# Performance work log

Measured on AMD Instinct MI355X. Metric: run time of the kernel, lower is better.

The kernel has to match this reference:

```python
import jax, jax.numpy as jnp
import numpy as np
import math

D = 1024
B, S = 4, 4096


def setup_inputs() -> dict:
    key = jax.random.key(0)
    ks = jax.random.split(key, 8)
    x = jax.random.normal(ks[0], (B, S, D), dtype=jnp.float32)
    W_omega = jax.random.normal(ks[1], (D, D), dtype=jnp.float32) * (1.0 / math.sqrt(D))
    b_omega = jnp.zeros((D,), dtype=jnp.float32)
    log_scale = jnp.full((D,), math.log(0.1), dtype=jnp.float32)
    ln_gamma = jnp.ones((4 * D,), dtype=jnp.float32)
    ln_beta = jnp.zeros((4 * D,), dtype=jnp.float32)
    W1 = jax.random.normal(ks[2], (4 * D, 2 * D), dtype=jnp.float32) * (1.0 / math.sqrt(4 * D))
    b1 = jnp.zeros((2 * D,), dtype=jnp.float32)
    W2 = jax.random.normal(ks[3], (2 * D, D), dtype=jnp.float32) * (1.0 / math.sqrt(2 * D))
    b2 = jnp.zeros((D,), dtype=jnp.float32)
    return {"x": x, "W_omega": W_omega, "b_omega": b_omega, "log_scale": log_scale,
            "ln_gamma": ln_gamma, "ln_beta": ln_beta, "W1": W1, "b1": b1, "W2": W2, "b2": b2}


def _layernorm(x, gamma, beta, eps=1e-5):
    mu = jnp.mean(x, axis=-1, keepdims=True)
    var = jnp.var(x, axis=-1, keepdims=True)
    return (x - mu) * jax.lax.rsqrt(var + eps) * gamma + beta


def reference(x, W_omega, b_omega, log_scale, ln_gamma, ln_beta, W1, b1, W2, b2):
    # x: (B, S, D)
    seq_len = x.shape[1]
    omega = jnp.einsum('bsd,de->bse', x, W_omega) + b_omega
    position = jnp.arange(1, seq_len + 1, dtype=x.dtype)[None, :, None]  # (1,S,1)
    pos_scale = 1.0 / jnp.sqrt(position)
    scale = jnp.exp(log_scale)
    omega_scaled = omega * scale * pos_scale
    phi = jnp.cumsum(omega_scaled, axis=1)
    cos_phi = jnp.cos(phi)
    sin_phi = jnp.sin(phi)
    content_real = x * cos_phi
    content_imag = x * sin_phi
    mem_real = jnp.cumsum(content_real, axis=1) / position
    mem_imag = jnp.cumsum(content_imag, axis=1) / position
    retrieved_real = mem_real * cos_phi + mem_imag * sin_phi
    retrieved_imag = mem_imag * cos_phi - mem_real * sin_phi
    context = jnp.concatenate([content_real, content_imag, retrieved_real, retrieved_imag], axis=-1)
    h = _layernorm(context, ln_gamma, ln_beta)
    h = jnp.einsum('bsf,fg->bsg', h, W1) + b1
    h = jax.nn.gelu(h, approximate=False)  # torch GELU default is exact erf
    # dropout is identity in eval mode
    phase_contribution = jnp.einsum('bsg,gd->bsd', h, W2) + b2
    return x + phase_contribution
```

## Files before the change

### kernel.cpp

```cpp
#include <hip/hip_runtime.h>
#include <hip/hip_bf16.h>
#include <math.h>

typedef __hip_bfloat16 bf16;
typedef __attribute__((ext_vector_type(8))) short bf16x8;
typedef __attribute__((ext_vector_type(4))) float f32x4;

static constexpr int DD = 1024;
static constexpr int BB = 4;
static constexpr int SS = 4096;
static constexpr int FD = 4096;
static constexpr int GDIM = 2048;
static constexpr long SD = (long)SS * DD;
static constexpr long SD4 = 4 * SD;

__device__ __forceinline__ void gl2lds16(const bf16* g, bf16* l) {
    __builtin_amdgcn_global_load_lds(
        (const __attribute__((address_space(1))) void*)g,
        (__attribute__((address_space(3))) void*)l, 16, 0, 0);
}

__device__ __forceinline__ float gelu_exact(float v) {
    const float ax = fabsf(v) * 0.70710678118654752f;
    const float t = 1.0f / (1.0f + 0.3275911f * ax);
    const float poly = t * (0.254829592f + t * (-0.284496736f +
                       t * (1.421413741f + t * (-1.453152027f + t * 1.061405429f))));
    const float er = 1.0f - poly * __expf(-ax * ax);
    const float erfv = v < 0.f ? -er : er;
    return 0.5f * v * (1.0f + erfv);
}

__device__ __forceinline__ float bf2f(unsigned short us) {
    return __uint_as_float(((unsigned)us) << 16);
}

template <int EPI>
__global__ __launch_bounds__(512, 2) void gemm256(
    const bf16* __restrict__ A, const bf16* __restrict__ BT, void* __restrict__ Cp,
    const float* __restrict__ bias, const float* __restrict__ Xadd,
    const float2* __restrict__ is2, const float* __restrict__ uArr,
    const float* __restrict__ tArr,
    int M, int N, int K, long strA, long strBT, long strC)
{
    extern __shared__ bf16 lds[];
    const int tid = threadIdx.x;
    const int l = tid & 63, wv = tid >> 6;
    const int wr = wv >> 2, wc = wv & 3;

    int lin = blockIdx.y * gridDim.x + blockIdx.x;
    {
        const int nwg = gridDim.x * gridDim.y;
        const int qq = nwg >> 3, rr = nwg & 7;
        const int xcd = lin & 7, idx = lin >> 3;
        lin = (xcd < rr ? xcd * (qq + 1) : rr * (qq + 1) + (xcd - rr) * qq) + idx;
    }
    const long m0 = (long)(lin / gridDim.x) * 256;
    const long n0 = (long)(lin % gridDim.x) * 256;

    A += (long)blockIdx.z * strA;
    BT += (long)blockIdx.z * strBT;

    const int schunk = (tid & 3) ^ ((tid >> 3) & 3);
    const bf16* pa = A + (m0 + (tid >> 2)) * (long)K + schunk * 8;
    const bf16* pb = BT + (n0 + (tid >> 2)) * (long)K + schunk * 8;
    const long rowK = 128L * (long)K;
    const int stgOff = wv * 512;

    const int fm = l & 15, q = l >> 4;
    const int lof = fm * 32 + ((q ^ ((fm >> 1) & 3)) * 8);

    f32x4 acc[8][4];
#pragma unroll
    for (int i = 0; i < 8; ++i)
#pragma unroll
        for (int j = 0; j < 4; ++j) acc[i][j] = (f32x4){0.f, 0.f, 0.f, 0.f};

    const int NT = K >> 6;

    {
        bf16* dA0 = lds + stgOff;
        bf16* dA1 = lds + 8192 + stgOff;
        bf16* dB0 = lds + 32768 + stgOff;
        bf16* dB1 = lds + 40960 + stgOff;
        gl2lds16(pa, dA0);       gl2lds16(pa + rowK, dA0 + 4096);
        gl2lds16(pb, dB0);       gl2lds16(pb + rowK, dB0 + 4096);
        gl2lds16(pa + 32, dA1);  gl2lds16(pa + 32 + rowK, dA1 + 4096);
        gl2lds16(pb + 32, dB1);  gl2lds16(pb + 32 + rowK, dB1 + 4096);
        asm volatile("s_waitcnt vmcnt(4)" ::: "memory");
        __builtin_amdgcn_s_barrier();
    }

    for (int t = 0; t < NT; ++t) {
        const int buf = t & 1;
        const bool more = (t + 1) < NT;
        const long ko = (long)(t + 1) * 64;
        const bf16* As0 = lds + buf * 16384;
        const bf16* As1 = As0 + 8192;
        const bf16* Bs0 = lds + 32768 + buf * 16384;
        const bf16* Bs1 = Bs0 + 8192;
        bf16* nA0 = lds + (buf ^ 1) * 16384 + stgOff;
        bf16* nA1 = nA0 + 8192;
        bf16* nB0 = lds + 32768 + (buf ^ 1) * 16384 + stgOff;
        bf16* nB1 = nB0 + 8192;

        {
            const bf16* bb = Bs0 + (wc * 64) * 32 + lof;
            const bf16* ab = As0 + (wr * 128) * 32 + lof;
            bf16x8 bq[4], a0[4], a1[4];
#pragma unroll
            for (int j = 0; j < 4; ++j) bq[j] = *(const bf16x8*)(bb + j * 512);
#pragma unroll
            for (int i = 0; i < 4; ++i) a0[i] = *(const bf16x8*)(ab + i * 512);
#pragma unroll
            for (int i = 0; i < 4; ++i) a1[i] = *(const bf16x8*)(ab + 64 * 32 + i * 512);
            if (more) {
                gl2lds16(pa + ko, nA0); gl2lds16(pa + ko + rowK, nA0 + 4096);
                gl2lds16(pb + ko, nB0); gl2lds16(pb + ko + rowK, nB0 + 4096);
            }
            __builtin_amdgcn_s_setprio(1);
#pragma unroll
            for (int i = 0; i < 4; ++i)
#pragma unroll
                for (int j = 0; j < 4; ++j)
                    acc[i][j] = __builtin_amdgcn_mfma_f32_16x16x32_bf16(a0[i], bq[j], acc[i][j], 0, 0, 0);
            __builtin_amdgcn_s_setprio(0);
            if (more) { gl2lds16(pa + ko + 32, nA1); gl2lds16(pa + ko + 32 + rowK, nA1 + 4096); }
            __builtin_amdgcn_s_setprio(1);
#pragma unroll
            for (int i = 0; i < 4; ++i)
#pragma unroll
                for (int j = 0; j < 4; ++j)
                    acc[4 + i][j] = __builtin_amdgcn_mfma_f32_16x16x32_bf16(a1[i], bq[j], acc[4 + i][j], 0, 0, 0);
            __builtin_amdgcn_s_setprio(0);
        }
        if (more) asm volatile("s_waitcnt vmcnt(6)" ::: "memory");
        else      asm volatile("s_waitcnt vmcnt(0)" ::: "memory");
        __builtin_amdgcn_s_barrier();

        {
            const bf16* bb = Bs1 + (wc * 64) * 32 + lof;
            const bf16* ab = As1 + (wr * 128) * 32 + lof;
            bf16x8 bq[4], a0[4], a1[4];
#pragma unroll
            for (int j = 0; j < 4; ++j) bq[j] = *(const bf16x8*)(bb + j * 512);
#pragma unroll
            for (int i = 0; i < 4; ++i) a0[i] = *(const bf16x8*)(ab + i * 512);
#pragma unroll
            for (int i = 0; i < 4; ++i) a1[i] = *(const bf16x8*)(ab + 64 * 32 + i * 512);
            if (more) { gl2lds16(pb + ko + 32, nB1); gl2lds16(pb + ko + 32 + rowK, nB1 + 4096); }
            __builtin_amdgcn_s_setprio(1);
#pragma unroll
            for (int i = 0; i < 4; ++i)
#pragma unroll
                for (int j = 0; j < 4; ++j)
                    acc[i][j] = __builtin_amdgcn_mfma_f32_16x16x32_bf16(a0[i], bq[j], acc[i][j], 0, 0, 0);
            __builtin_amdgcn_s_setprio(0);
            __builtin_amdgcn_s_setprio(1);
#pragma unroll
            for (int i = 0; i < 4; ++i)
#pragma unroll
                for (int j = 0; j < 4; ++j)
                    acc[4 + i][j] = __builtin_amdgcn_mfma_f32_16x16x32_bf16(a1[i], bq[j], acc[4 + i][j], 0, 0, 0);
            __builtin_amdgcn_s_setprio(0);
        }
        if (more) {
            asm volatile("s_waitcnt vmcnt(4)" ::: "memory");
            __builtin_amdgcn_s_barrier();
        }
    }

    const long cb = (long)blockIdx.z * strC;
    float uu[4], tb[4];
    if (EPI == 1) {
#pragma unroll
        for (int j = 0; j < 4; ++j) {
            const long col = n0 + wc * 64 + j * 16 + fm;
            uu[j] = uArr[col];
            tb[j] = tArr[col] + bias[col];
        }
    }
#pragma unroll
    for (int i = 0; i < 8; ++i) {
        const long rB = m0 + wr * 128 + i * 16 + q * 4;
#pragma unroll
        for (int r2 = 0; r2 < 4; ++r2) {
            const long row = rB + r2;
            float2 st;
            if (EPI == 1) st = is2[row];
#pragma unroll
            for (int j = 0; j < 4; ++j) {
                const long col = n0 + wc * 64 + j * 16 + fm;
                float v = acc[i][j][r2];
                if (EPI == 0) {
                    v += bias[row];
                    ((bf16*)Cp)[cb + row * (long)N + col] = __float2bfloat16(v);
                } else if (EPI == 1) {
                    v = st.x * v - st.y * uu[j] + tb[j];
                    v = gelu_exact(v);
                    ((bf16*)Cp)[cb + row * (long)N + col] = __float2bfloat16(v);
                } else {
                    v += bias[col] + Xadd[row * (long)N + col];
                    ((float*)Cp)[cb + row * (long)N + col] = v;
                }
            }
        }
    }
}

__global__ void conv_bf16(const float* __restrict__ in, bf16* __restrict__ out, long n) {
    long i = ((long)blockIdx.x * 256 + threadIdx.x) * 4;
    if (i >= n) return;
    const float4 v = *(const float4*)(in + i);
    bf16 o[4] = {__float2bfloat16(v.x), __float2bfloat16(v.y),
                 __float2bfloat16(v.z), __float2bfloat16(v.w)};
    *(uint2*)(out + i) = *(uint2*)o;
}

__global__ void transpose_f32_bf16(const float* __restrict__ in, bf16* __restrict__ out,
                                   int R, int C, long inStr, long outStr,
                                   const float* __restrict__ rscale) {
    __shared__ float tl[64][65];
    const float* ip = in + (long)blockIdx.z * inStr;
    bf16* op = out + (long)blockIdx.z * outStr;
    const int r0 = blockIdx.y * 64, c0 = blockIdx.x * 64;
    const int tr = threadIdx.x >> 6, tc = threadIdx.x & 63;
#pragma unroll
    for (int k = 0; k < 16; k++) {
        int r = k * 4 + tr;
        float v = ip[(long)(r0 + r) * C + c0 + tc];
        if (rscale) v *= rscale[r0 + r];
        tl[r][tc] = v;
    }
    __syncthreads();
#pragma unroll
    for (int k = 0; k < 16; k++) {
        int r = k * 4 + tr;
        op[(long)(c0 + r) * R + r0 + tc] = __float2bfloat16(tl[tc][r]);
    }
}

__global__ void zero_f32(float* p, int n) {
    int i = blockIdx.x * 256 + threadIdx.x;
    if (i < n) p[i] = 0.f;
}

__global__ void ut_kernel(const float* __restrict__ W1, const float* __restrict__ gamma,
                          const float* __restrict__ beta, float* __restrict__ uArr,
                          float* __restrict__ tArr) {
    const int g = blockIdx.x * 256 + threadIdx.x;
    const int f0 = blockIdx.y * 512;
    float su = 0.f, st = 0.f;
    for (int f = 0; f < 512; ++f) {
        const float w = W1[(long)(f0 + f) * GDIM + g];
        su += gamma[f0 + f] * w;
        st += beta[f0 + f] * w;
    }
    atomicAdd(&uArr[g], su);
    atomicAdd(&tArr[g], st);
}

__global__ __launch_bounds__(512) void scan8(
    const bf16* __restrict__ omegaT, const bf16* __restrict__ xT,
    const float* __restrict__ log_scale, bf16* __restrict__ ctx,
    long strIn, long strCtx)
{
    __shared__ float stA[8], stB[8], stC[8];
    const int d = blockIdx.x;
    const int z = blockIdx.z;
    const int wv = threadIdx.x >> 6, lane = threadIdx.x & 63;
    const float sc = expf(log_scale[d]);
    const bf16* po = omegaT + (long)z * strIn + (long)d * SS;
    const bf16* px = xT + (long)z * strIn + (long)d * SS;
    bf16* pc = ctx + (long)z * strCtx + (long)d * SS;

    const int s0 = wv * 512;
    float phi_loc[8], xv[8], cph[8], sph[8], crs[8], cis[8];

    float lphi = 0.f;
#pragma unroll
    for (int c = 0; c < 8; ++c) {
        const int s = s0 + c * 64 + lane;
        const float pos = (float)(s + 1);
        float w = __bfloat162float(po[s]) * sc * rsqrtf(pos);
        xv[c] = __bfloat162float(px[s]);
#pragma unroll
        for (int dlt = 1; dlt < 64; dlt <<= 1) {
            float v = __shfl_up(w, dlt, 64);
            if (lane >= dlt) w += v;
        }
        phi_loc[c] = lphi + w;
        lphi += __shfl(w, 63, 64);
    }
    if (lane == 0) stA[wv] = lphi;
    __syncthreads();
    float phi_off = 0.f;
#pragma unroll
    for (int u = 0; u < 8; ++u) phi_off += (u < wv) ? stA[u] : 0.f;

    float lcr = 0.f, lci = 0.f;
#pragma unroll
    for (int c = 0; c < 8; ++c) {
        const float phi = phi_loc[c] + phi_off;
        float sp, cp;
        sincosf(phi, &sp, &cp);
        cph[c] = cp; sph[c] = sp;
        float a = xv[c] * cp, b = xv[c] * sp;
#pragma unroll
        for (int dlt = 1; dlt < 64; dlt <<= 1) {
            float v1 = __shfl_up(a, dlt, 64);
            float v2 = __shfl_up(b, dlt, 64);
            if (lane >= dlt) { a += v1; b += v2; }
        }
        crs[c] = lcr + a;
        cis[c] = lci + b;
        lcr += __shfl(a, 63, 64);
        lci += __shfl(b, 63, 64);
    }
    if (lane == 0) { stB[wv] = lcr; stC[wv] = lci; }
    __syncthreads();
    float roff = 0.f, ioff = 0.f;
#pragma unroll
    for (int u = 0; u < 8; ++u) {
        roff += (u < wv) ? stB[u] : 0.f;
        ioff += (u < wv) ? stC[u] : 0.f;
    }

#pragma unroll
    for (int c = 0; c < 8; ++c) {
        const int s = s0 + c * 64 + lane;
        const float invp = 1.0f / (float)(s + 1);
        const float mr = (crs[c] + roff) * invp;
        const float mi = (cis[c] + ioff) * invp;
        const float cp = cph[c], sp = sph[c];
        const float cr = xv[c] * cp, ci = xv[c] * sp;
        const float rr = mr * cp + mi * sp;
        const float ri = mi * cp - mr * sp;
        pc[s] = __float2bfloat16(cr);
        pc[(long)DD * SS + s] = __float2bfloat16(ci);
        pc[2L * DD * SS + s] = __float2bfloat16(rr);
        pc[3L * DD * SS + s] = __float2bfloat16(ri);
    }
}

__global__ __launch_bounds__(256) void tpair(bf16* __restrict__ ctx, long strCtx) {
    __shared__ float tA[64][65];
    __shared__ float tB[64][65];
    const int z = blockIdx.z;
    int rem = blockIdx.x, a = 0;
    for (int i = 0; i < 64; i++) {
        int cnt = 64 - i;
        if (rem < cnt) { a = i; break; }
        rem -= cnt;
    }
    const int b = a + rem;
    bf16* base = ctx + (long)z * strCtx;
    const int tr = threadIdx.x >> 6, tc = threadIdx.x & 63;
#pragma unroll
    for (int k = 0; k < 16; k++) {
        int i = k * 4 + tr;
        tA[i][tc] = __bfloat162float(base[(long)(a * 64 + i) * 4096 + b * 64 + tc]);
    }
    if (a != b) {
#pragma unroll
        for (int k = 0; k < 16; k++) {
            int i = k * 4 + tr;
            tB[i][tc] = __bfloat162float(base[(long)(b * 64 + i) * 4096 + a * 64 + tc]);
        }
    }
    __syncthreads();
#pragma unroll
    for (int k = 0; k < 16; k++) {
        int i = k * 4 + tr;
        base[(long)(b * 64 + i) * 4096 + a * 64 + tc] = __float2bfloat16(tA[tc][i]);
    }
    if (a != b) {
#pragma unroll
        for (int k = 0; k < 16; k++) {
            int i = k * 4 + tr;
            base[(long)(a * 64 + i) * 4096 + b * 64 + tc] = __float2bfloat16(tB[tc][i]);
        }
    }
}

__global__ __launch_bounds__(256) void stats2(
    const bf16* __restrict__ ctx, float2* __restrict__ is2, long strCtx)
{
    const int s = blockIdx.x * 4 + (threadIdx.x >> 6);
    const int lane = threadIdx.x & 63;
    const int z = blockIdx.z;
    const bf16* p = ctx + (long)z * strCtx + (long)s * FD;
    float sm = 0.f, sq = 0.f;
#pragma unroll
    for (int i = 0; i < 8; ++i) {
        bf16x8 v8 = *(const bf16x8*)(p + lane * 8 + i * 512);
#pragma unroll
        for (int j = 0; j < 8; ++j) {
            const float v = bf2f((unsigned short)v8[j]);
            sm += v;
            sq += v * v;
        }
    }
#pragma unroll
    for (int o = 1; o < 64; o <<= 1) {
        sm += __shfl_xor(sm, o, 64);
        sq += __shfl_xor(sq, o, 64);
    }
    if (lane == 0) {
        const float mu = sm * (1.0f / FD);
        const float var = sq * (1.0f / FD) - mu * mu;
        const float is = rsqrtf(var + 1e-5f);
        is2[z * SS + s] = make_float2(is, is * mu);
    }
}

extern "C" void kernel_launch(void* const* d_in, const int* in_sizes, int n_in,
                              void* d_out, int out_size, void* d_ws, size_t ws_size,
                              hipStream_t stream)
{
    const float* x = (const float*)d_in[0];
    const float* Wo = (const float*)d_in[1];
    const float* bo = (const float*)d_in[2];
    const float* lsc = (const float*)d_in[3];
    const float* gam = (const float*)d_in[4];
    const float* bet = (const float*)d_in[5];
    const float* W1 = (const float*)d_in[6];
    const float* b1 = (const float*)d_in[7];
    const float* W2 = (const float*)d_in[8];
    const float* b2 = (const float*)d_in[9];

    static bool attr_done = false;
    if (!attr_done) {
        hipFuncSetAttribute(reinterpret_cast<const void*>(gemm256<0>),
                            hipFuncAttributeMaxDynamicSharedMemorySize, 131072);
        hipFuncSetAttribute(reinterpret_cast<const void*>(gemm256<1>),
                            hipFuncAttributeMaxDynamicSharedMemorySize, 131072);
        hipFuncSetAttribute(reinterpret_cast<const void*>(gemm256<2>),
                            hipFuncAttributeMaxDynamicSharedMemorySize, 131072);
        attr_done = true;
    }

    char* ws = (char*)d_ws;
    const size_t MB = 1024 * 1024;

    bf16* W1gT = (bf16*)(ws + 0);
    bf16* W2T = (bf16*)(ws + 16 * MB);
    bf16* WoT = (bf16*)(ws + 20 * MB);
    float2* is2 = (float2*)(ws + 22 * MB);
    float* uArr = (float*)(ws + 22 * MB + 128 * 1024);
    float* tArr = (float*)(ws + 22 * MB + 136 * 1024);

    transpose_f32_bf16<<<dim3(DD / 64, DD / 64, 1), 256, 0, stream>>>(Wo, WoT, DD, DD, 0, 0, nullptr);
    transpose_f32_bf16<<<dim3(GDIM / 64, FD / 64, 1), 256, 0, stream>>>(W1, W1gT, FD, GDIM, 0, 0, gam);
    transpose_f32_bf16<<<dim3(DD / 64, GDIM / 64, 1), 256, 0, stream>>>(W2, W2T, GDIM, DD, 0, 0, nullptr);
    zero_f32<<<(2 * GDIM + 255) / 256, 256, 0, stream>>>(uArr, 2 * GDIM);
    ut_kernel<<<dim3(GDIM / 256, FD / 512, 1), 256, 0, stream>>>(W1, gam, bet, uArr, tArr);

    const int NPAIR = 64 * 65 / 2;

    if (ws_size >= 220 * MB) {
        bf16* xT  = (bf16*)(ws + 23 * MB);
        bf16* omT = (bf16*)(ws + 55 * MB);
        bf16* ctx = (bf16*)(ws + 87 * MB);
        bf16* xb  = (bf16*)(ws + 87 * MB);
        bf16* h1  = (bf16*)(ws + 23 * MB);

        conv_bf16<<<(int)(BB * SD / 1024), 256, 0, stream>>>(x, xb, BB * SD);
        transpose_f32_bf16<<<dim3(DD / 64, SS / 64, BB), 256, 0, stream>>>(x, xT, SS, DD, SD, SD, nullptr);

        gemm256<0><<<dim3(SS / 256, DD / 256, BB), 512, 131072, stream>>>(
            WoT, xb, omT, bo, nullptr, nullptr, nullptr, nullptr, DD, SS, DD, 0L, SD, SD);

        scan8<<<dim3(DD, 1, BB), 512, 0, stream>>>(omT, xT, lsc, ctx, SD, SD4);

        tpair<<<dim3(NPAIR, 1, BB), 256, 0, stream>>>(ctx, SD4);

        stats2<<<dim3(SS / 4, 1, BB), 256, 0, stream>>>(ctx, is2, SD4);

        gemm256<1><<<dim3(GDIM / 256, BB * SS / 256, 1), 512, 131072, stream>>>(
            ctx, W1gT, h1, b1, nullptr, is2, uArr, tArr, BB * SS, GDIM, FD, 0L, 0L, 0L);

        gemm256<2><<<dim3(DD / 256, BB * SS / 256, 1), 512, 131072, stream>>>(
            h1, W2T, d_out, b2, x, nullptr, nullptr, nullptr, BB * SS, DD, GDIM, 0L, 0L, 0L);
    } else {
        bf16* xb  = (bf16*)(ws + 23 * MB);
        bf16* ctx = (bf16*)(ws + 23 * MB);
        bf16* omT = (bf16*)(ws + 55 * MB);
        bf16* xT  = (bf16*)(ws + 63 * MB);
        bf16* h1  = (bf16*)(ws + 55 * MB);

        for (int b = 0; b < BB; b++) {
            const float* xbf = x + (long)b * SD;
            conv_bf16<<<(int)(SD / 1024), 256, 0, stream>>>(xbf, xb, SD);
            transpose_f32_bf16<<<dim3(DD / 64, SS / 64, 1), 256, 0, stream>>>(xbf, xT, SS, DD, 0, 0, nullptr);
            gemm256<0><<<dim3(SS / 256, DD / 256, 1), 512, 131072, stream>>>(
                WoT, xb, omT, bo, nullptr, nullptr, nullptr, nullptr, DD, SS, DD, 0L, 0L, 0L);
            scan8<<<dim3(DD, 1, 1), 512, 0, stream>>>(omT, xT, lsc, ctx, 0L, 0L);
            tpair<<<dim3(NPAIR, 1, 1), 256, 0, stream>>>(ctx, 0L);
            stats2<<<dim3(SS / 4, 1, 1), 256, 0, stream>>>(ctx, is2, 0L);
            gemm256<1><<<dim3(GDIM / 256, SS / 256, 1), 512, 131072, stream>>>(
                ctx, W1gT, h1, b1, nullptr, is2, uArr, tArr, SS, GDIM, FD, 0L, 0L, 0L);
            gemm256<2><<<dim3(DD / 256, SS / 256, 1), 512, 131072, stream>>>(
                h1, W2T, (float*)d_out + (long)b * SD, b2, xbf, nullptr, nullptr, nullptr,
                SS, DD, GDIM, 0L, 0L, 0L);
        }
    }
}
```

Baseline: 709.6 us.

## Fuse layernorm stats into transpose and merge x conversion kernels

Removes the separate stats2 kernel: the tpair transpose now computes per-row sum and sum of squares with wave reductions and atomically accumulates them. The GEMM1 epilogue turns these into mean and inverse std. The bf16 conversion and transpose of x are merged into one xprep kernel so x is read once, and ut_kernel gets more blocks over a shorter loop. In exchange there are many more atomics, an extra zeroing kernel, and slightly different float summation order.

```diff
diff --git a/kernel.cpp b/kernel.cpp
--- a/kernel.cpp
+++ b/kernel.cpp
@@ -38,7 +38,7 @@
 __global__ __launch_bounds__(512, 2) void gemm256(
     const bf16* __restrict__ A, const bf16* __restrict__ BT, void* __restrict__ Cp,
     const float* __restrict__ bias, const float* __restrict__ Xadd,
-    const float2* __restrict__ is2, const float* __restrict__ uArr,
+    const float2* __restrict__ s2, const float* __restrict__ uArr,
     const float* __restrict__ tArr,
     int M, int N, int K, long strA, long strBT, long strC)
 {
@@ -185,8 +185,14 @@
 #pragma unroll
         for (int r2 = 0; r2 < 4; ++r2) {
             const long row = rB + r2;
-            float2 st;
-            if (EPI == 1) st = is2[row];
+            float isv = 0.f, ismu = 0.f;
+            if (EPI == 1) {
+                const float2 st = s2[row];
+                const float mu = st.x * (1.0f / FD);
+                const float var = st.y * (1.0f / FD) - mu * mu;
+                isv = rsqrtf(var + 1e-5f);
+                ismu = isv * mu;
+            }
 #pragma unroll
             for (int j = 0; j < 4; ++j) {
                 const long col = n0 + wc * 64 + j * 16 + fm;
@@ -195,7 +201,7 @@
                     v += bias[row];
                     ((bf16*)Cp)[cb + row * (long)N + col] = __float2bfloat16(v);
                 } else if (EPI == 1) {
-                    v = st.x * v - st.y * uu[j] + tb[j];
+                    v = isv * v - ismu * uu[j] + tb[j];
                     v = gelu_exact(v);
                     ((bf16*)Cp)[cb + row * (long)N + col] = __float2bfloat16(v);
                 } else {
@@ -207,13 +213,29 @@
     }
 }
 
-__global__ void conv_bf16(const float* __restrict__ in, bf16* __restrict__ out, long n) {
-    long i = ((long)blockIdx.x * 256 + threadIdx.x) * 4;
-    if (i >= n) return;
-    const float4 v = *(const float4*)(in + i);
-    bf16 o[4] = {__float2bfloat16(v.x), __float2bfloat16(v.y),
-                 __float2bfloat16(v.z), __float2bfloat16(v.w)};
-    *(uint2*)(out + i) = *(uint2*)o;
+__global__ __launch_bounds__(256) void xprep(
+    const float* __restrict__ in, bf16* __restrict__ xb, bf16* __restrict__ xT,
+    long inStr, long outStr)
+{
+    __shared__ float tl[64][65];
+    const float* ip = in + (long)blockIdx.z * inStr;
+    bf16* ob = xb + (long)blockIdx.z * outStr;
+    bf16* ot = xT + (long)blockIdx.z * outStr;
+    const int r0 = blockIdx.y * 64, c0 = blockIdx.x * 64;
+    const int tr = threadIdx.x >> 6, tc = threadIdx.x & 63;
+#pragma unroll
+    for (int k = 0; k < 16; k++) {
+        int r = k * 4 + tr;
+        float v = ip[(long)(r0 + r) * DD + c0 + tc];
+        tl[r][tc] = v;
+        ob[(long)(r0 + r) * DD + c0 + tc] = __float2bfloat16(v);
+    }
+    __syncthreads();
+#pragma unroll
+    for (int k = 0; k < 16; k++) {
+        int r = k * 4 + tr;
+        ot[(long)(c0 + r) * SS + r0 + tc] = __float2bfloat16(tl[tc][r]);
+    }
 }
 
 __global__ void transpose_f32_bf16(const float* __restrict__ in, bf16* __restrict__ out,
@@ -248,9 +270,9 @@
                           const float* __restrict__ beta, float* __restrict__ uArr,
                           float* __restrict__ tArr) {
     const int g = blockIdx.x * 256 + threadIdx.x;
-    const int f0 = blockIdx.y * 512;
+    const int f0 = blockIdx.y * 128;
     float su = 0.f, st = 0.f;
-    for (int f = 0; f < 512; ++f) {
+    for (int f = 0; f < 128; ++f) {
         const float w = W1[(long)(f0 + f) * GDIM + g];
         su += gamma[f0 + f] * w;
         st += beta[f0 + f] * w;
@@ -342,7 +364,8 @@
     }
 }
 
-__global__ __launch_bounds__(256) void tpair(bf16* __restrict__ ctx, long strCtx) {
+__global__ __launch_bounds__(256) void tpair(bf16* __restrict__ ctx, long strCtx,
+                                             float2* __restrict__ s2) {
     __shared__ float tA[64][65];
     __shared__ float tB[64][65];
     const int z = blockIdx.z;
@@ -354,6 +377,7 @@
     }
     const int b = a + rem;
     bf16* base = ctx + (long)z * strCtx;
+    float2* s2z = s2 + (long)z * SS;
     const int tr = threadIdx.x >> 6, tc = threadIdx.x & 63;
 #pragma unroll
     for (int k = 0; k < 16; k++) {
@@ -371,45 +395,36 @@
 #pragma unroll
     for (int k = 0; k < 16; k++) {
         int i = k * 4 + tr;
-        base[(long)(b * 64 + i) * 4096 + a * 64 + tc] = __float2bfloat16(tA[tc][i]);
+        const float v = tA[tc][i];
+        base[(long)(b * 64 + i) * 4096 + a * 64 + tc] = __float2bfloat16(v);
+        float sm = v, sq = v * v;
+#pragma unroll
+        for (int o = 1; o < 64; o <<= 1) {
+            sm += __shfl_xor(sm, o, 64);
+            sq += __shfl_xor(sq, o, 64);
+        }
+        if (tc == 0) {
+            atomicAdd(&s2z[b * 64 + i].x, sm);
+            atomicAdd(&s2z[b * 64 + i].y, sq);
+        }
     }
     if (a != b) {
 #pragma unroll
         for (int k = 0; k < 16; k++) {
             int i = k * 4 + tr;
-            base[(long)(a * 64 + i) * 4096 + b * 64 + tc] = __float2bfloat16(tB[tc][i]);
-        }
-    }
-}
-
-__global__ __launch_bounds__(256) void stats2(
-    const bf16* __restrict__ ctx, float2* __restrict__ is2, long strCtx)
-{
-    const int s = blockIdx.x * 4 + (threadIdx.x >> 6);
-    const int lane = threadIdx.x & 63;
-    const int z = blockIdx.z;
-    const bf16* p = ctx + (long)z * strCtx + (long)s * FD;
-    float sm = 0.f, sq = 0.f;
-#pragma unroll
-    for (int i = 0; i < 8; ++i) {
-        bf16x8 v8 = *(const bf16x8*)(p + lane * 8 + i * 512);
-#pragma unroll
-        for (int j = 0; j < 8; ++j) {
-            const float v = bf2f((unsigned short)v8[j]);
-            sm += v;
-            sq += v * v;
-        }
-    }
-#pragma unroll
-    for (int o = 1; o < 64; o <<= 1) {
-        sm += __shfl_xor(sm, o, 64);
-        sq += __shfl_xor(sq, o, 64);
-    }
-    if (lane == 0) {
-        const float mu = sm * (1.0f / FD);
-        const float var = sq * (1.0f / FD) - mu * mu;
-        const float is = rsqrtf(var + 1e-5f);
-        is2[z * SS + s] = make_float2(is, is * mu);
+            const float v = tB[tc][i];
+            base[(long)(a * 64 + i) * 4096 + b * 64 + tc] = __float2bfloat16(v);
+            float sm = v, sq = v * v;
+#pragma unroll
+            for (int o = 1; o < 64; o <<= 1) {
+                sm += __shfl_xor(sm, o, 64);
+                sq += __shfl_xor(sq, o, 64);
+            }
+            if (tc == 0) {
+                atomicAdd(&s2z[a * 64 + i].x, sm);
+                atomicAdd(&s2z[a * 64 + i].y, sq);
+            }
+        }
     }
 }
 
@@ -445,7 +460,7 @@
     bf16* W1gT = (bf16*)(ws + 0);
     bf16* W2T = (bf16*)(ws + 16 * MB);
     bf16* WoT = (bf16*)(ws + 20 * MB);
-    float2* is2 = (float2*)(ws + 22 * MB);
+    float2* s2 = (float2*)(ws + 22 * MB);
     float* uArr = (float*)(ws + 22 * MB + 128 * 1024);
     float* tArr = (float*)(ws + 22 * MB + 136 * 1024);
 
@@ -453,7 +468,7 @@
     transpose_f32_bf16<<<dim3(GDIM / 64, FD / 64, 1), 256, 0, stream>>>(W1, W1gT, FD, GDIM, 0, 0, gam);
     transpose_f32_bf16<<<dim3(DD / 64, GDIM / 64, 1), 256, 0, stream>>>(W2, W2T, GDIM, DD, 0, 0, nullptr);
     zero_f32<<<(2 * GDIM + 255) / 256, 256, 0, stream>>>(uArr, 2 * GDIM);
-    ut_kernel<<<dim3(GDIM / 256, FD / 512, 1), 256, 0, stream>>>(W1, gam, bet, uArr, tArr);
+    ut_kernel<<<dim3(GDIM / 256, FD / 128, 1), 256, 0, stream>>>(W1, gam, bet, uArr, tArr);
 
     const int NPAIR = 64 * 65 / 2;
 
@@ -464,20 +479,19 @@
         bf16* xb  = (bf16*)(ws + 87 * MB);
         bf16* h1  = (bf16*)(ws + 23 * MB);
 
-        conv_bf16<<<(int)(BB * SD / 1024), 256, 0, stream>>>(x, xb, BB * SD);
-        transpose_f32_bf16<<<dim3(DD / 64, SS / 64, BB), 256, 0, stream>>>(x, xT, SS, DD, SD, SD, nullptr);
+        xprep<<<dim3(DD / 64, SS / 64, BB), 256, 0, stream>>>(x, xb, xT, SD, SD);
+
+        zero_f32<<<(2 * BB * SS + 255) / 256, 256, 0, stream>>>((float*)s2, 2 * BB * SS);
 
         gemm256<0><<<dim3(SS / 256, DD / 256, BB), 512, 131072, stream>>>(
             WoT, xb, omT, bo, nullptr, nullptr, nullptr, nullptr, DD, SS, DD, 0L, SD, SD);
 
         scan8<<<dim3(DD, 1, BB), 512, 0, stream>>>(omT, xT, lsc, ctx, SD, SD4);
 
-        tpair<<<dim3(NPAIR, 1, BB), 256, 0, stream>>>(ctx, SD4);
-
-        stats2<<<dim3(SS / 4, 1, BB), 256, 0, stream>>>(ctx, is2, SD4);
+        tpair<<<dim3(NPAIR, 1, BB), 256, 0, stream>>>(ctx, SD4, s2);
 
         gemm256<1><<<dim3(GDIM / 256, BB * SS / 256, 1), 512, 131072, stream>>>(
-            ctx, W1gT, h1, b1, nullptr, is2, uArr, tArr, BB * SS, GDIM, FD, 0L, 0L, 0L);
+            ctx, W1gT, h1, b1, nullptr, s2, uArr, tArr, BB * SS, GDIM, FD, 0L, 0L, 0L);
 
         gemm256<2><<<dim3(DD / 256, BB * SS / 256, 1), 512, 131072, stream>>>(
             h1, W2T, d_out, b2, x, nullptr, nullptr, nullptr, BB * SS, DD, GDIM, 0L, 0L, 0L);
@@ -490,15 +504,14 @@
 
         for (int b = 0; b < BB; b++) {
             const float* xbf = x + (long)b * SD;
-            conv_bf16<<<(int)(SD / 1024), 256, 0, stream>>>(xbf, xb, SD);
-            transpose_f32_bf16<<<dim3(DD / 64, SS / 64, 1), 256, 0, stream>>>(xbf, xT, SS, DD, 0, 0, nullptr);
+            xprep<<<dim3(DD / 64, SS / 64, 1), 256, 0, stream>>>(xbf, xb, xT, 0L, 0L);
+            zero_f32<<<(2 * SS + 255) / 256, 256, 0, stream>>>((float*)s2, 2 * SS);
             gemm256<0><<<dim3(SS / 256, DD / 256, 1), 512, 131072, stream>>>(
                 WoT, xb, omT, bo, nullptr, nullptr, nullptr, nullptr, DD, SS, DD, 0L, 0L, 0L);
             scan8<<<dim3(DD, 1, 1), 512, 0, stream>>>(omT, xT, lsc, ctx, 0L, 0L);
-            tpair<<<dim3(NPAIR, 1, 1), 256, 0, stream>>>(ctx, 0L);
-            stats2<<<dim3(SS / 4, 1, 1), 256, 0, stream>>>(ctx, is2, 0L);
+            tpair<<<dim3(NPAIR, 1, 1), 256, 0, stream>>>(ctx, 0L, s2);
             gemm256<1><<<dim3(GDIM / 256, SS / 256, 1), 512, 131072, stream>>>(
-                ctx, W1gT, h1, b1, nullptr, is2, uArr, tArr, SS, GDIM, FD, 0L, 0L, 0L);
+                ctx, W1gT, h1, b1, nullptr, s2, uArr, tArr, SS, GDIM, FD, 0L, 0L, 0L);
             gemm256<2><<<dim3(DD / 256, SS / 256, 1), 512, 131072, stream>>>(
                 h1, W2T, (float*)d_out + (long)b * SD, b2, xbf, nullptr, nullptr, nullptr,
                 SS, DD, GDIM, 0L, 0L, 0L);
```

New measurement: 845.2 us. 19.1% more time.
